# Kernel tuning notes

Hardware: AMD Instinct MI355X
Metric: run time of the kernel (lower is better)

## Reference

```python
import jax, jax.numpy as jnp
import numpy as np

NUM_CLASSES = 10
OUTPUT_DIM = 128
HIDDEN_DIM = 64


def setup_inputs() -> dict:
    key = jax.random.key(0)
    k1, k2, k3, k4, k5, k6 = jax.random.split(key, 6)
    B, S, F = 16, 4096, 512
    X_support = jax.random.normal(k1, (B, S, F), dtype=jnp.float32)
    y_support = jax.random.randint(k2, (B, S), 0, NUM_CLASSES, dtype=jnp.int32)
    # MLP params: Linear(6, HIDDEN) -> GELU -> Linear(HIDDEN, OUTPUT)
    w1 = jax.random.normal(k3, (6, HIDDEN_DIM), dtype=jnp.float32) * (1.0 / np.sqrt(6.0))
    b1 = jax.random.normal(k4, (HIDDEN_DIM,), dtype=jnp.float32) * 0.01
    w2 = jax.random.normal(k5, (HIDDEN_DIM, OUTPUT_DIM), dtype=jnp.float32) * (1.0 / np.sqrt(HIDDEN_DIM))
    b2 = jax.random.normal(k6, (OUTPUT_DIM,), dtype=jnp.float32) * 0.01
    return {"X_support": X_support, "y_support": y_support,
            "w1": w1, "b1": b1, "w2": w2, "b2": b2}


def _feature_target_stats(X, y):
    """Vectorized equivalent of FeatureTargetStatsEncoder per-(batch,feature) loops.
    X: [B, S, F] float, y: [B, S] int class labels. Returns stats [B, F, 6]."""
    B, S, F = X.shape
    missing_rate = jnp.isnan(X).astype(X.dtype).mean(axis=1)           # [B, F]
    Xc = jnp.nan_to_num(X, nan=0.0)
    gmean = Xc.mean(axis=1)                                            # [B, F]
    variance = Xc.var(axis=1)                                          # biased (unbiased=False)
    absX = jnp.abs(Xc)
    mean_abs = absX.mean(axis=1)
    max_abs = absX.max(axis=1)
    # unique_ratio: count distinct values per (b, f) via sort + diff
    xs = jnp.sort(Xc, axis=1)
    n_unique = 1.0 + (jnp.diff(xs, axis=1) != 0).astype(Xc.dtype).sum(axis=1)
    unique_ratio = n_unique / S
    # classification target score: between-class variance / overall variance
    onehot = jax.nn.one_hot(y, NUM_CLASSES, dtype=Xc.dtype)            # [B, S, C]
    counts = onehot.sum(axis=1)                                        # [B, C]
    csum = jnp.einsum('bsc,bsf->bcf', onehot, Xc)                      # [B, C, F]
    cmean = csum / jnp.maximum(counts, 1.0)[:, :, None]
    dev2 = (cmean - gmean[:, None, :]) ** 2
    between = (counts[:, :, None] * dev2).sum(axis=1) / jnp.maximum(counts.sum(axis=1), 1.0)[:, None]
    target_score = between / jnp.maximum(variance, 1e-6)
    stats = jnp.stack([target_score, missing_rate, unique_ratio,
                       variance, mean_abs, max_abs], axis=-1)          # [B, F, 6]
    return jnp.nan_to_num(stats, nan=0.0, posinf=0.0, neginf=0.0)


def reference(X_support, y_support, w1, b1, w2, b2):
    stats = _feature_target_stats(X_support, y_support)                # [B, F, 6]
    h = jax.nn.gelu(stats @ w1 + b1, approximate=False)               # exact GELU like nn.GELU()
    return h @ w2 + b2                                                 # [B, F, OUTPUT_DIM]
```

## Files before the change

### kernel.cpp

```cpp
#include <hip/hip_runtime.h>
#include <math.h>

#define NS 4096
#define NF 512
#define NB 16
#define NC 10
#define HSIZE 8192
#define HMASK 8191
#define HEMPTY 0xFFFFFFFFu
#define TSR 128
#define TSC 16
#define NSEG 4
#define SEGR (NS / NSEG)
#define WS_P_OFF  1024
#define P2_BYTES (NB * NF * NSEG * 16 * 4)
#define WS_XT_OFF (WS_P_OFF + P2_BYTES)

__device__ __forceinline__ float wave_reduce_add(float v) {
    #pragma unroll
    for (int off = 32; off > 0; off >>= 1) v += __shfl_down(v, off, 64);
    return v;
}

__device__ __forceinline__ unsigned int pat_of(float x) {
    if (x != x) x = 0.f;
    unsigned int p = __float_as_uint(x);
    return (p == 0x80000000u) ? 0u : p;
}

__launch_bounds__(512, 4)
__global__ void stripe_stats_kernel(const float* __restrict__ X,
                                    float* __restrict__ XT,
                                    const int* __restrict__ y,
                                    float* __restrict__ P2,
                                    int* __restrict__ counts_i) {
    __shared__ float t[2][TSR][TSC + 1];
    __shared__ int ys[2][TSR];
    __shared__ int hist[NC];
    const int b   = blockIdx.x;
    const int f0  = blockIdx.y * TSC;
    const int seg = blockIdx.z;
    const int tid = threadIdx.x;
    const bool do_hist = (blockIdx.y == 0);
    if (do_hist && tid < NC) hist[tid] = 0;

    const int lrow = tid >> 2, lq = tid & 3;
    const int col  = tid >> 5, rq = tid & 31;

    const int sbase = seg * SEGR;
    const float* Xb = X + (size_t)b * NS * NF + f0 + lq * 4;
    const int*   yb = y + (size_t)b * NS;
    float* XTc = XT + ((size_t)b * NF + f0 + col) * NS;

    float sum = 0.f, sumsq = 0.f, sumabs = 0.f, maxabs = 0.f, nancnt = 0.f;
    float csum[NC];
    #pragma unroll
    for (int c = 0; c < NC; c++) csum[c] = 0.f;

    {
        const float4 xc = *(const float4*)(Xb + (size_t)(sbase + lrow) * NF);
        t[0][lrow][lq * 4 + 0] = xc.x; t[0][lrow][lq * 4 + 1] = xc.y;
        t[0][lrow][lq * 4 + 2] = xc.z; t[0][lrow][lq * 4 + 3] = xc.w;
        if (tid < TSR / 4) {
            const int4 y4 = *(const int4*)(yb + sbase + tid * 4);
            ys[0][tid * 4 + 0] = y4.x; ys[0][tid * 4 + 1] = y4.y;
            ys[0][tid * 4 + 2] = y4.z; ys[0][tid * 4 + 3] = y4.w;
        }
    }

    for (int it = 0; it < SEGR / TSR; ++it) {
        const int cur = it & 1;
        const int s0 = sbase + it * TSR;
        const bool more = (it + 1 < SEGR / TSR);
        float4 xn = make_float4(0.f, 0.f, 0.f, 0.f);
        int4 yn4 = make_int4(0, 0, 0, 0);
        if (more) {
            xn = *(const float4*)(Xb + (size_t)(s0 + TSR + lrow) * NF);
            if (tid < TSR / 4) yn4 = *(const int4*)(yb + s0 + TSR + tid * 4);
        }
        __syncthreads();
        if (do_hist && tid < TSR) atomicAdd(&hist[ys[cur][tid]], 1);

        #pragma unroll
        for (int j = 0; j < 4; j++) {
            const int r = rq + 32 * j;
            const float raw = t[cur][r][col];
            const int yc = ys[cur][r];
            XTc[s0 + r] = raw;
            float x = raw;
            if (x != x) { nancnt += 1.f; x = 0.f; }
            sum += x;
            sumsq = fmaf(x, x, sumsq);
            const float a = fabsf(x);
            sumabs += a;
            maxabs = fmaxf(maxabs, a);
            #pragma unroll
            for (int c = 0; c < NC; c++) csum[c] += (yc == c) ? x : 0.f;
        }
        if (more) {
            const int nb = cur ^ 1;
            t[nb][lrow][lq * 4 + 0] = xn.x; t[nb][lrow][lq * 4 + 1] = xn.y;
            t[nb][lrow][lq * 4 + 2] = xn.z; t[nb][lrow][lq * 4 + 3] = xn.w;
            if (tid < TSR / 4) {
                ys[nb][tid * 4 + 0] = yn4.x; ys[nb][tid * 4 + 1] = yn4.y;
                ys[nb][tid * 4 + 2] = yn4.z; ys[nb][tid * 4 + 3] = yn4.w;
            }
        }
    }

    float st[15] = { sum, sumsq, sumabs, nancnt, maxabs,
                     csum[0], csum[1], csum[2], csum[3], csum[4],
                     csum[5], csum[6], csum[7], csum[8], csum[9] };
    #pragma unroll
    for (int s = 0; s < 15; s++) {
        float v = st[s];
        #pragma unroll
        for (int off = 16; off > 0; off >>= 1) {
            const float o = __shfl_down(v, off, 32);
            v = (s == 4) ? fmaxf(v, o) : v + o;
        }
        if (rq == 0)
            P2[(((size_t)b * NF + f0 + col) * NSEG + seg) * 16 + s] = v;
    }
    if (do_hist) {
        __syncthreads();
        if (tid < NC) atomicAdd(&counts_i[b * NC + tid], hist[tid]);
    }
}

__launch_bounds__(512, 8)
__global__ void fused_hash_mlp(const float* __restrict__ XT,
                               const float* __restrict__ P2,
                               const int* __restrict__ counts_i,
                               const float* __restrict__ w1,
                               const float* __restrict__ b1,
                               const float* __restrict__ w2,
                               const float* __restrict__ b2,
                               float* __restrict__ out) {
    __shared__ __align__(16) unsigned int T[HSIZE];
    __shared__ int anyflag;

    const int w = blockIdx.x;
    const int g = (w & 7) * 1024 + (w >> 3);
    const int b = g >> 9;
    const int f = g & (NF - 1);
    const int tid = threadIdx.x;
    const int wave = tid >> 6, lane = tid & 63;

    const float4* Xc4 = (const float4*)(XT + ((size_t)b * NF + f) * NS);
    const float4 xa = Xc4[tid];
    const float4 xb = Xc4[512 + tid];

    uint4* h4 = (uint4*)T;
    const uint4 e4 = make_uint4(HEMPTY, HEMPTY, HEMPTY, HEMPTY);
    #pragma unroll
    for (int i = 0; i < HSIZE / 4 / 512; i++) h4[i * 512 + tid] = e4;
    __syncthreads();

    unsigned int pat[8] = { pat_of(xa.x), pat_of(xa.y), pat_of(xa.z), pat_of(xa.w),
                            pat_of(xb.x), pat_of(xb.y), pat_of(xb.z), pat_of(xb.w) };
    unsigned int slot[8];
    #pragma unroll
    for (int e = 0; e < 8; e++) slot[e] = (pat[e] * 2654435761u) >> 19;

    float uniq = 0.f;
    int uns = 0xFF;
    for (;;) {
        #pragma unroll
        for (int e = 0; e < 8; e++)
            if (uns & (1 << e)) T[slot[e]] = pat[e];
        __syncthreads();
        int matched = 0;
        #pragma unroll
        for (int e = 0; e < 8; e++)
            if (uns & (1 << e)) matched |= (T[slot[e]] == pat[e]) ? (1 << e) : 0;
        __syncthreads();
        if (tid == 0) anyflag = 0;
        #pragma unroll
        for (int e = 0; e < 8; e++)
            if (matched & (1 << e)) T[slot[e]] = 0x7FC00000u | (unsigned)(tid * 8 + e);
        __syncthreads();
        #pragma unroll
        for (int e = 0; e < 8; e++)
            if (matched & (1 << e))
                uniq += (T[slot[e]] == (0x7FC00000u | (unsigned)(tid * 8 + e))) ? 1.f : 0.f;
        uns &= ~matched;
        #pragma unroll
        for (int e = 0; e < 8; e++)
            if (uns & (1 << e))
                slot[e] = (slot[e] + ((pat[e] & 0x1FFFu) | 1u)) & HMASK;
        if (uns) anyflag = 1;
        __syncthreads();
        if (!anyflag) break;
    }

    float* r = (float*)T;
    float* stats_s = r + 32;
    float* h_s = r + 64;

    uniq = wave_reduce_add(uniq);
    if (lane == 0) r[wave] = uniq;
    __syncthreads();

    if (tid == 0) {
        float u = 0.f;
        #pragma unroll
        for (int i = 0; i < 8; i++) u += r[i];
        const float* Pp = P2 + ((size_t)b * NF + f) * (NSEG * 16);
        float S[15];
        #pragma unroll
        for (int s = 0; s < 15; s++) {
            float v0 = Pp[s], v1 = Pp[16 + s], v2 = Pp[32 + s], v3 = Pp[48 + s];
            S[s] = (s == 4) ? fmaxf(fmaxf(v0, v1), fmaxf(v2, v3))
                            : (v0 + v1) + (v2 + v3);
        }
        const float invS = 1.f / (float)NS;
        const float gmean    = S[0] * invS;
        const float variance = fmaxf(S[1] * invS - gmean * gmean, 0.f);
        const float mean_abs = S[2] * invS;
        const float missing  = S[3] * invS;
        const float max_abs  = S[4];
        float between = 0.f;
        #pragma unroll
        for (int c = 0; c < NC; c++) {
            const float cnt = (float)counts_i[b * NC + c];
            const float cm  = S[5 + c] / fmaxf(cnt, 1.f);
            const float d   = cm - gmean;
            between = fmaf(cnt * d, d, between);
        }
        between *= invS;
        const float target = between / fmaxf(variance, 1e-6f);
        float st6[6] = { target, missing, u * invS, variance, mean_abs, max_abs };
        #pragma unroll
        for (int i = 0; i < 6; i++) {
            float v = st6[i];
            if (!(fabsf(v) < INFINITY)) v = 0.f;
            stats_s[i] = v;
        }
    }
    __syncthreads();

    if (tid < 64) {
        float z = b1[tid];
        #pragma unroll
        for (int i = 0; i < 6; i++) z = fmaf(stats_s[i], w1[i * 64 + tid], z);
        h_s[tid] = 0.5f * z * (1.f + erff(z * 0.70710678118654752440f));
    }
    __syncthreads();
    if (tid < 128) {
        float o = b2[tid];
        #pragma unroll
        for (int j = 0; j < 64; j++) o = fmaf(h_s[j], w2[j * 128 + tid], o);
        out[(size_t)g * 128 + tid] = o;
    }
}

__global__ void count_classes_kernel(const int* __restrict__ y, float* __restrict__ counts) {
    __shared__ int hist[NC];
    const int b = blockIdx.x;
    if (threadIdx.x < NC) hist[threadIdx.x] = 0;
    __syncthreads();
    for (int s = threadIdx.x; s < NS; s += blockDim.x)
        atomicAdd(&hist[y[b * NS + s]], 1);
    __syncthreads();
    if (threadIdx.x < NC) counts[b * NC + threadIdx.x] = (float)hist[threadIdx.x];
}

__device__ __forceinline__ float wave_reduce_max64(float v) {
    #pragma unroll
    for (int off = 32; off > 0; off >>= 1) v = fmaxf(v, __shfl_down(v, off, 64));
    return v;
}

__launch_bounds__(256)
__global__ void fused_stats_mlp_kernel(const float* __restrict__ X,
                                       const int* __restrict__ y,
                                       const float* __restrict__ counts,
                                       const float* __restrict__ w1,
                                       const float* __restrict__ b1,
                                       const float* __restrict__ w2,
                                       const float* __restrict__ b2,
                                       float* __restrict__ out) {
    __shared__ unsigned int hash[HSIZE];
    __shared__ float red[4][16];
    __shared__ float stats_s[6];
    __shared__ float h_s[64];

    const int w = blockIdx.x;
    const int g = (w & 7) * 1024 + (w >> 3);
    const int b = g >> 9;
    const int f = g & (NF - 1);
    const int tid = threadIdx.x;

    #pragma unroll
    for (int i = 0; i < HSIZE / 256; i++) hash[tid + i * 256] = HEMPTY;
    __syncthreads();

    const float* Xp = X + (size_t)b * NS * NF + f;
    const int*   yp = y + b * NS;

    float sum = 0.f, sumsq = 0.f, sumabs = 0.f, maxabs = 0.f, nancnt = 0.f, uniq = 0.f;
    float csum[NC];
    #pragma unroll
    for (int c = 0; c < NC; c++) csum[c] = 0.f;

    #pragma unroll
    for (int k0 = 0; k0 < 16; k0 += 8) {
        float xv[8]; int yv[8];
        #pragma unroll
        for (int k = 0; k < 8; k++) {
            const int s = (k0 + k) * 256 + tid;
            xv[k] = Xp[(size_t)s * NF];
            yv[k] = yp[s];
        }
        #pragma unroll
        for (int k = 0; k < 8; k++) {
            float x = xv[k];
            if (x != x) { nancnt += 1.f; x = 0.f; }
            sum += x;
            sumsq = fmaf(x, x, sumsq);
            const float a = fabsf(x);
            sumabs += a;
            maxabs = fmaxf(maxabs, a);
            const int yc = yv[k];
            #pragma unroll
            for (int c = 0; c < NC; c++) csum[c] += (yc == c) ? x : 0.f;
            unsigned int pat = __float_as_uint(x);
            if (pat == 0x80000000u) pat = 0u;
            unsigned int slot = (pat * 2654435761u) >> 19;
            for (;;) {
                const unsigned int old = atomicCAS(&hash[slot], HEMPTY, pat);
                if (old == HEMPTY) { uniq += 1.f; break; }
                if (old == pat) break;
                slot = (slot + 1) & HMASK;
            }
        }
    }

    sum    = wave_reduce_add(sum);
    sumsq  = wave_reduce_add(sumsq);
    sumabs = wave_reduce_add(sumabs);
    nancnt = wave_reduce_add(nancnt);
    uniq   = wave_reduce_add(uniq);
    maxabs = wave_reduce_max64(maxabs);
    #pragma unroll
    for (int c = 0; c < NC; c++) csum[c] = wave_reduce_add(csum[c]);

    const int wave = tid >> 6, lane = tid & 63;
    if (lane == 0) {
        red[wave][0] = sum;    red[wave][1] = sumsq; red[wave][2] = sumabs;
        red[wave][3] = nancnt; red[wave][4] = uniq;  red[wave][5] = maxabs;
        #pragma unroll
        for (int c = 0; c < NC; c++) red[wave][6 + c] = csum[c];
    }
    __syncthreads();

    if (tid == 0) {
        float t[16];
        #pragma unroll
        for (int v = 0; v < 16; v++) t[v] = red[0][v];
        #pragma unroll
        for (int wv = 1; wv < 4; wv++) {
            #pragma unroll
            for (int v = 0; v < 16; v++) {
                if (v == 5) t[v] = fmaxf(t[v], red[wv][v]);
                else        t[v] += red[wv][v];
            }
        }
        const float invS = 1.f / (float)NS;
        const float gmean    = t[0] * invS;
        const float variance = fmaxf(t[1] * invS - gmean * gmean, 0.f);
        const float mean_abs = t[2] * invS;
        const float missing  = t[3] * invS;
        const float n_unique = t[4];
        const float max_abs  = t[5];
        float between = 0.f;
        #pragma unroll
        for (int c = 0; c < NC; c++) {
            const float cnt = counts[b * NC + c];
            const float cm  = t[6 + c] / fmaxf(cnt, 1.f);
            const float d   = cm - gmean;
            between += cnt * d * d;
        }
        between *= invS;
        const float target = between / fmaxf(variance, 1e-6f);
        float st[6] = { target, missing, n_unique * invS, variance, mean_abs, max_abs };
        #pragma unroll
        for (int i = 0; i < 6; i++) {
            float v = st[i];
            if (!(fabsf(v) < INFINITY)) v = 0.f;
            stats_s[i] = v;
        }
    }
    __syncthreads();

    if (tid < 64) {
        float z = b1[tid];
        #pragma unroll
        for (int i = 0; i < 6; i++) z = fmaf(stats_s[i], w1[i * 64 + tid], z);
        h_s[tid] = 0.5f * z * (1.f + erff(z * 0.70710678118654752440f));
    }
    __syncthreads();
    if (tid < 128) {
        float o = b2[tid];
        #pragma unroll
        for (int j = 0; j < 64; j++) o = fmaf(h_s[j], w2[j * 128 + tid], o);
        out[(size_t)g * 128 + tid] = o;
    }
}

extern "C" void kernel_launch(void* const* d_in, const int* in_sizes, int n_in,
                              void* d_out, int out_size, void* d_ws, size_t ws_size,
                              hipStream_t stream) {
    const float* X  = (const float*)d_in[0];
    const int*   y  = (const int*)d_in[1];
    const float* w1 = (const float*)d_in[2];
    const float* b1 = (const float*)d_in[3];
    const float* w2 = (const float*)d_in[4];
    const float* b2 = (const float*)d_in[5];
    float* out = (float*)d_out;

    const size_t xt_bytes = (size_t)NB * NF * NS * sizeof(float);
    if (ws_size >= (size_t)WS_XT_OFF + xt_bytes) {
        int*   counts_i = (int*)d_ws;
        float* P2 = (float*)((char*)d_ws + WS_P_OFF);
        float* XT = (float*)((char*)d_ws + WS_XT_OFF);
        hipMemsetAsync(d_ws, 0, NB * NC * sizeof(int), stream);
        stripe_stats_kernel<<<dim3(NB, NF / TSC, NSEG), 512, 0, stream>>>(
            X, XT, y, P2, counts_i);
        fused_hash_mlp<<<NB * NF, 512, 0, stream>>>(
            XT, P2, counts_i, w1, b1, w2, b2, out);
    } else {
        float* counts = (float*)d_ws;
        count_classes_kernel<<<NB, 256, 0, stream>>>(y, counts);
        fused_stats_mlp_kernel<<<NB * NF, 256, 0, stream>>>(X, y, counts, w1, b1, w2, b2, out);
    }
}
```

Before: 311.5 us.

## Simplify hash-based unique counting to two barriers per probe round

```diff
diff --git a/kernel.cpp b/kernel.cpp
--- a/kernel.cpp
+++ b/kernel.cpp
@@ -72,13 +72,16 @@
         const int cur = it & 1;
         const int s0 = sbase + it * TSR;
         const bool more = (it + 1 < SEGR / TSR);
+
+        __syncthreads();
+
         float4 xn = make_float4(0.f, 0.f, 0.f, 0.f);
         int4 yn4 = make_int4(0, 0, 0, 0);
         if (more) {
             xn = *(const float4*)(Xb + (size_t)(s0 + TSR + lrow) * NF);
             if (tid < TSR / 4) yn4 = *(const int4*)(yb + s0 + TSR + tid * 4);
         }
-        __syncthreads();
+
         if (do_hist && tid < TSR) atomicAdd(&hist[ys[cur][tid]], 1);
 
         #pragma unroll
@@ -138,7 +141,6 @@
                                const float* __restrict__ b2,
                                float* __restrict__ out) {
     __shared__ __align__(16) unsigned int T[HSIZE];
-    __shared__ int anyflag;
 
     const int w = blockIdx.x;
     const int g = (w & 7) * 1024 + (w >> 3);
@@ -159,40 +161,41 @@
 
     unsigned int pat[8] = { pat_of(xa.x), pat_of(xa.y), pat_of(xa.z), pat_of(xa.w),
                             pat_of(xb.x), pat_of(xb.y), pat_of(xb.z), pat_of(xb.w) };
-    unsigned int slot[8];
-    #pragma unroll
-    for (int e = 0; e < 8; e++) slot[e] = (pat[e] * 2654435761u) >> 19;
+    unsigned int slot[8], step[8];
+    #pragma unroll
+    for (int e = 0; e < 8; e++) {
+        slot[e] = (pat[e] * 2654435761u) >> 19;
+        step[e] = (pat[e] & 0x1FFFu) | 1u;
+    }
+
+    int uns = 0xFF;
+    int wr  = 0xFF;
+    for (;;) {
+        #pragma unroll
+        for (int e = 0; e < 8; e++)
+            if (wr & (1 << e)) T[slot[e]] = pat[e];
+        __syncthreads();
+        int newwr = 0;
+        #pragma unroll
+        for (int e = 0; e < 8; e++) {
+            if (uns & (1 << e)) {
+                const unsigned int v = T[slot[e]];
+                if (v == pat[e])       uns &= ~(1 << e);
+                else if (v == HEMPTY)  newwr |= (1 << e);
+                else                   slot[e] = (slot[e] + step[e]) & HMASK;
+            }
+        }
+        wr = newwr;
+        if (__syncthreads_count(uns) == 0) break;
+    }
 
     float uniq = 0.f;
-    int uns = 0xFF;
-    for (;;) {
-        #pragma unroll
-        for (int e = 0; e < 8; e++)
-            if (uns & (1 << e)) T[slot[e]] = pat[e];
-        __syncthreads();
-        int matched = 0;
-        #pragma unroll
-        for (int e = 0; e < 8; e++)
-            if (uns & (1 << e)) matched |= (T[slot[e]] == pat[e]) ? (1 << e) : 0;
-        __syncthreads();
-        if (tid == 0) anyflag = 0;
-        #pragma unroll
-        for (int e = 0; e < 8; e++)
-            if (matched & (1 << e)) T[slot[e]] = 0x7FC00000u | (unsigned)(tid * 8 + e);
-        __syncthreads();
-        #pragma unroll
-        for (int e = 0; e < 8; e++)
-            if (matched & (1 << e))
-                uniq += (T[slot[e]] == (0x7FC00000u | (unsigned)(tid * 8 + e))) ? 1.f : 0.f;
-        uns &= ~matched;
-        #pragma unroll
-        for (int e = 0; e < 8; e++)
-            if (uns & (1 << e))
-                slot[e] = (slot[e] + ((pat[e] & 0x1FFFu) | 1u)) & HMASK;
-        if (uns) anyflag = 1;
-        __syncthreads();
-        if (!anyflag) break;
-    }
+    #pragma unroll
+    for (int i = 0; i < 4; i++) {
+        const uint4 v = h4[i * 512 + tid];
+        uniq += (v.x != HEMPTY) + (v.y != HEMPTY) + (v.z != HEMPTY) + (v.w != HEMPTY);
+    }
+    __syncthreads();
 
     float* r = (float*)T;
     float* stats_s = r + 32;
```

Measured after the change: 410.9 us. +31.9%, slower.
